# Performance work log

Measured on AMD Instinct MI355X. Metric: run time of the kernel, lower is better.

## Reference

```python
import jax, jax.numpy as jnp
import numpy as np

NUM_HEADS = 8

def _l2norm(t, eps=1e-12):
    # F.normalize(p=2, dim=-1) with eps clamp
    n = jnp.sqrt(jnp.sum(t * t, axis=-1, keepdims=True))
    return t / jnp.maximum(n, eps)

def setup_inputs() -> dict:
    key = jax.random.key(0)
    ks = jax.random.split(key, 4)
    B, N, C = 16, 3136, 768
    x = jax.random.normal(ks[0], (B, N, C), dtype=jnp.float32)
    W_qkv = jax.random.normal(ks[1], (C, 3 * C), dtype=jnp.float32) * (1.0 / np.sqrt(C))
    temp = jnp.ones((NUM_HEADS, 1, 1), dtype=jnp.float32)
    W_proj = jax.random.normal(ks[2], (C, C), dtype=jnp.float32) * (1.0 / np.sqrt(C))
    b_proj = jnp.zeros((C,), dtype=jnp.float32)
    return {"x": x, "W_qkv": W_qkv, "temp": temp, "W_proj": W_proj, "b_proj": b_proj}

def reference(x, W_qkv, temp, W_proj, b_proj):
    B, N, C = x.shape
    h = NUM_HEADS
    d = C // h
    qkv = (x @ W_qkv).reshape(B, N, 3, h, d)
    qkv = jnp.transpose(qkv, (2, 0, 3, 1, 4))  # [3,B,h,N,d]
    q, k, v = qkv[0], qkv[1], qkv[2]           # [B,h,N,d]
    # transpose to channel-major: [B,h,d,N]
    q = jnp.swapaxes(q, -2, -1)
    k = jnp.swapaxes(k, -2, -1)
    v = jnp.swapaxes(v, -2, -1)
    q = _l2norm(q)
    k = _l2norm(k)
    # attn = k @ q^T over token dim: [B,h,d,d]
    attn = jnp.einsum('bhcn,bhen->bhce', k, q)
    attn = attn * temp  # temp broadcasts [h,1,1]
    attn = jax.nn.softmax(attn, axis=-1)
    out = jnp.einsum('bhce,bhen->bhcn', attn, v)  # [B,h,d,N]
    out = jnp.transpose(out, (0, 3, 1, 2)).reshape(B, N, C)
    return out @ W_proj + b_proj
```

## Files before the change

### kernel.cpp

```cpp
#include <hip/hip_runtime.h>

using bf16x8 = __attribute__((ext_vector_type(8))) __bf16;
using f32x4  = __attribute__((ext_vector_type(4))) float;

#define AS1 __attribute__((address_space(1)))
#define AS3 __attribute__((address_space(3)))

__device__ __forceinline__ unsigned short f2bf(float f) {
    unsigned int x = __float_as_uint(f);
    x += 0x7fffu + ((x >> 16) & 1u);
    return (unsigned short)(x >> 16);
}

__device__ __forceinline__ int xcd_remap(int orig, int nwg) {
    int q = nwg >> 3, r = nwg & 7;
    int xcd = orig & 7, lin = orig >> 3;
    return (xcd < r ? xcd * (q + 1) : r * (q + 1) + (xcd - r) * q) + lin;
}

__global__ void cvt_f32_bf16_kernel(const float4* __restrict__ in, ushort4* __restrict__ out, int n4) {
    int stride = gridDim.x * blockDim.x;
    for (int i = blockIdx.x * blockDim.x + threadIdx.x; i < n4; i += stride) {
        float4 v = in[i];
        ushort4 o;
        o.x = f2bf(v.x); o.y = f2bf(v.y); o.z = f2bf(v.z); o.w = f2bf(v.w);
        out[i] = o;
    }
}

__global__ void transpose_f32_bf16_kernel(const float* __restrict__ W, unsigned short* __restrict__ Wt,
                                          int K, int N) {
    __shared__ float tile[32][33];
    int n0 = blockIdx.x << 5, k0 = blockIdx.y << 5;
    int tx = threadIdx.x, ty = threadIdx.y;
#pragma unroll
    for (int i = 0; i < 32; i += 8)
        tile[ty + i][tx] = W[(size_t)(k0 + ty + i) * N + (n0 + tx)];
    __syncthreads();
#pragma unroll
    for (int i = 0; i < 32; i += 8)
        Wt[(size_t)(n0 + ty + i) * K + (k0 + tx)] = f2bf(tile[tx][ty + i]);
}

__device__ __forceinline__ void stage_tile_128x64(const unsigned short* g, int ldK,
                                                  unsigned short* lds, int tid) {
#pragma unroll
    for (int r = 0; r < 4; ++r) {
        int i = (r << 8) + tid;
        int row = i >> 3;
        int colb = (i & 7) << 4;
        int srcb = row * (ldK << 1) + (colb ^ ((row & 7) << 4));
        __builtin_amdgcn_global_load_lds(
            (AS1 unsigned int*)(unsigned long long)((const char*)g + srcb),
            (AS3 unsigned int*)((char*)lds + (i << 4)),
            16, 0, 0);
    }
}

__device__ __forceinline__ bf16x8 lds_read_swz(const unsigned short* base, int row, int kbyte) {
    int off = (row << 7) + (kbyte ^ ((row & 7) << 4));
    return *(const bf16x8*)((const char*)base + off);
}

__global__ __launch_bounds__(256, 2)
void gemm_bt_kernel(const unsigned short* __restrict__ A, const unsigned short* __restrict__ Bt,
                    unsigned short* __restrict__ obf, int M, int N, int K, int ntx) {
    __shared__ unsigned short As[128 * 64];
    __shared__ unsigned short Bs[128 * 64];
    int tid = threadIdx.x;
    int lane = tid & 63, w = tid >> 6;
    int wm = w >> 1, wn = w & 1;
    int wg = xcd_remap(blockIdx.x, gridDim.x);
    int bx = wg % ntx, by = wg / ntx;
    int m0 = by << 7, n0 = bx << 7;
    const unsigned short* Ag = A + (size_t)m0 * K;
    const unsigned short* Bg = Bt + (size_t)n0 * K;

    f32x4 zz = {0.f, 0.f, 0.f, 0.f};
    f32x4 acc[4][4];
#pragma unroll
    for (int a = 0; a < 4; ++a)
#pragma unroll
        for (int b = 0; b < 4; ++b) acc[a][b] = zz;

    for (int kb = 0; kb < K; kb += 64) {
        stage_tile_128x64(Ag + kb, K, As, tid);
        stage_tile_128x64(Bg + kb, K, Bs, tid);
        __syncthreads();
#pragma unroll
        for (int ks = 0; ks < 2; ++ks) {
            int kbyte = (ks << 6) + ((lane >> 4) << 4);
            bf16x8 af[4], bfr[4];
#pragma unroll
            for (int f = 0; f < 4; ++f)
                af[f] = lds_read_swz(As, (wm << 6) + (f << 4) + (lane & 15), kbyte);
#pragma unroll
            for (int f = 0; f < 4; ++f)
                bfr[f] = lds_read_swz(Bs, (wn << 6) + (f << 4) + (lane & 15), kbyte);
#pragma unroll
            for (int fm = 0; fm < 4; ++fm)
#pragma unroll
                for (int fn = 0; fn < 4; ++fn)
                    acc[fm][fn] = __builtin_amdgcn_mfma_f32_16x16x32_bf16(af[fm], bfr[fn], acc[fm][fn], 0, 0, 0);
        }
        __syncthreads();
    }

    int rbase = m0 + (wm << 6) + ((lane >> 4) << 2);
    int cbase = n0 + (wn << 6) + (lane & 15);
#pragma unroll
    for (int fm = 0; fm < 4; ++fm)
#pragma unroll
        for (int j = 0; j < 4; ++j) {
            size_t ro = (size_t)(rbase + (fm << 4) + j) * N;
#pragma unroll
            for (int fn = 0; fn < 4; ++fn)
                obf[ro + cbase + (fn << 4)] = f2bf(acc[fm][fn][j]);
        }
}

__global__ __launch_bounds__(256, 2)
void gemm_v_proj_kernel(const unsigned short* __restrict__ qkv, const unsigned short* __restrict__ MT,
                        float* __restrict__ out, const float* __restrict__ bias) {
    __shared__ unsigned short As[128 * 64];
    __shared__ unsigned short Bs[128 * 64];
    int tid = threadIdx.x;
    int lane = tid & 63, w = tid >> 6;
    int wm = w >> 1, wn = w & 1;
    int wg = xcd_remap(blockIdx.x, gridDim.x);
    int bx = wg % 6;
    int t2 = wg / 6;
    int mt = t2 % 25, b = t2 / 25;
    int m0 = mt << 7, n0 = bx << 7;
    const unsigned short* Ab = qkv + (size_t)b * 3136 * 2304 + 1536;
    const unsigned short* Bg = MT + (size_t)b * 589824 + (size_t)n0 * 768;

    f32x4 zz = {0.f, 0.f, 0.f, 0.f};
    f32x4 acc[4][4];
#pragma unroll
    for (int a = 0; a < 4; ++a)
#pragma unroll
        for (int c = 0; c < 4; ++c) acc[a][c] = zz;

    for (int kb = 0; kb < 768; kb += 64) {
#pragma unroll
        for (int r = 0; r < 4; ++r) {
            int i = (r << 8) + tid;
            int row = i >> 3, slot = i & 7;
            int rg = m0 + row; if (rg > 3135) rg = 3135;
            const char* src = (const char*)(Ab + (size_t)rg * 2304 + kb) + ((slot ^ (row & 7)) << 4);
            __builtin_amdgcn_global_load_lds(
                (AS1 unsigned int*)(unsigned long long)src,
                (AS3 unsigned int*)((char*)As + (i << 4)), 16, 0, 0);
        }
        stage_tile_128x64(Bg + kb, 768, Bs, tid);
        __syncthreads();
#pragma unroll
        for (int ks = 0; ks < 2; ++ks) {
            int kbyte = (ks << 6) + ((lane >> 4) << 4);
            bf16x8 af[4], bfr[4];
#pragma unroll
            for (int f = 0; f < 4; ++f)
                af[f] = lds_read_swz(As, (wm << 6) + (f << 4) + (lane & 15), kbyte);
#pragma unroll
            for (int f = 0; f < 4; ++f)
                bfr[f] = lds_read_swz(Bs, (wn << 6) + (f << 4) + (lane & 15), kbyte);
#pragma unroll
            for (int fm = 0; fm < 4; ++fm)
#pragma unroll
                for (int fn = 0; fn < 4; ++fn)
                    acc[fm][fn] = __builtin_amdgcn_mfma_f32_16x16x32_bf16(af[fm], bfr[fn], acc[fm][fn], 0, 0, 0);
        }
        __syncthreads();
    }

    int rloc = m0 + (wm << 6) + ((lane >> 4) << 2);
    int cbase = n0 + (wn << 6) + (lane & 15);
    float bv[4];
#pragma unroll
    for (int fn = 0; fn < 4; ++fn) bv[fn] = bias[cbase + (fn << 4)];
#pragma unroll
    for (int fm = 0; fm < 4; ++fm)
#pragma unroll
        for (int j = 0; j < 4; ++j) {
            int rr = rloc + (fm << 4) + j;
            if (rr < 3136) {
                size_t ro = ((size_t)b * 3136 + rr) * 768;
#pragma unroll
                for (int fn = 0; fn < 4; ++fn)
                    out[ro + cbase + (fn << 4)] = acc[fm][fn][j] + bv[fn];
            }
        }
}

__global__ __launch_bounds__(256)
void cov_mfma_kernel(const unsigned short* __restrict__ qkv, float* __restrict__ S,
                     float* __restrict__ qn2, float* __restrict__ kn2) {
    __shared__ unsigned short Kl[96 * 40];
    __shared__ unsigned short Ql[96 * 40];
    int bh = blockIdx.x;
    int b = bh >> 3, h = bh & 7;
    int tok0 = blockIdx.y * 448;
    int tid = threadIdx.x;
    int lane = tid & 63, w = tid >> 6;
    int wr = w & 1, wc = w >> 1;
    int rot = tid & 7;

    f32x4 zz = {0.f, 0.f, 0.f, 0.f};
    f32x4 acc[3][3];
#pragma unroll
    for (int a = 0; a < 3; ++a)
#pragma unroll
        for (int c = 0; c < 3; ++c) acc[a][c] = zz;
    float qn = 0.f, kn = 0.f;

    const uint4* qg = (const uint4*)qkv;

    for (int step = 0; step < 14; ++step) {
        int tokBase = b * 3136 + tok0 + (step << 5);
        __syncthreads();
#pragma unroll
        for (int r = 0; r < 3; ++r) {
            int idx = (r << 8) + tid;
            int isK = idx >= 384;
            int j = isK ? idx - 384 : idx;
            int tok = j / 12, c = j % 12;
            uint4 u = qg[(size_t)(tokBase + tok) * 288 + h * 12 + (isK ? 96 : 0) + c];
            unsigned short* dst = isK ? Kl : Ql;
            const unsigned short* us = (const unsigned short*)&u;
#pragma unroll
            for (int i = 0; i < 8; ++i) {
                int e = (i + rot) & 7;
                dst[(c * 8 + e) * 40 + tok] = us[e];
            }
        }
        __syncthreads();
        if (tid < 96) {
#pragma unroll
            for (int t = 0; t < 4; ++t) {
                bf16x8 v = *(const bf16x8*)((const char*)Ql + tid * 80 + (t << 4));
#pragma unroll
                for (int i = 0; i < 8; ++i) { float f = (float)v[i]; qn = fmaf(f, f, qn); }
            }
        } else if (tid >= 128 && tid < 224) {
            int c = tid - 128;
#pragma unroll
            for (int t = 0; t < 4; ++t) {
                bf16x8 v = *(const bf16x8*)((const char*)Kl + c * 80 + (t << 4));
#pragma unroll
                for (int i = 0; i < 8; ++i) { float f = (float)v[i]; kn = fmaf(f, f, kn); }
            }
        }
        int kbyte = (lane >> 4) << 4;
        bf16x8 af[3], bfv[3];
#pragma unroll
        for (int f = 0; f < 3; ++f)
            af[f] = *(const bf16x8*)((const char*)Kl + (wr * 48 + f * 16 + (lane & 15)) * 80 + kbyte);
#pragma unroll
        for (int f = 0; f < 3; ++f)
            bfv[f] = *(const bf16x8*)((const char*)Ql + (wc * 48 + f * 16 + (lane & 15)) * 80 + kbyte);
#pragma unroll
        for (int fm = 0; fm < 3; ++fm)
#pragma unroll
            for (int fn = 0; fn < 3; ++fn)
                acc[fm][fn] = __builtin_amdgcn_mfma_f32_16x16x32_bf16(af[fm], bfv[fn], acc[fm][fn], 0, 0, 0);
    }

    float* Sb = S + (size_t)bh * 9216;
    int rloc = wr * 48 + ((lane >> 4) << 2);
    int cloc = wc * 48 + (lane & 15);
#pragma unroll
    for (int fm = 0; fm < 3; ++fm)
#pragma unroll
        for (int fn = 0; fn < 3; ++fn)
#pragma unroll
            for (int j = 0; j < 4; ++j)
                atomicAdd(&Sb[(rloc + fm * 16 + j) * 96 + cloc + fn * 16], acc[fm][fn][j]);
    if (tid < 96) atomicAdd(&qn2[bh * 96 + tid], qn);
    if (tid >= 128 && tid < 224) atomicAdd(&kn2[bh * 96 + tid - 128], kn);
}

__global__ __launch_bounds__(128)
void softmax_kernel(const float* __restrict__ S, const float* __restrict__ qn2,
                    const float* __restrict__ kn2, const float* __restrict__ temp,
                    unsigned short* __restrict__ attnT) {
    int bh = blockIdx.x, h = bh & 7;
    __shared__ float Sl[96 * 97];
    __shared__ float qinv[96];
    int tid = threadIdx.x;
    const float* Sg = S + (size_t)bh * 9216;
    for (int i = tid; i < 9216; i += 128) Sl[(i / 96) * 97 + (i % 96)] = Sg[i];
    if (tid < 96) qinv[tid] = 1.f / fmaxf(sqrtf(qn2[bh * 96 + tid]), 1e-12f);
    __syncthreads();
    if (tid < 96) {
        int c = tid;
        float scale = (1.f / fmaxf(sqrtf(kn2[bh * 96 + c]), 1e-12f)) * temp[h];
        float* row = &Sl[c * 97];
        float mx = -3.4e38f;
        for (int e = 0; e < 96; ++e) {
            float v = row[e] * scale * qinv[e];
            row[e] = v;
            mx = fmaxf(mx, v);
        }
        float s = 0.f;
        for (int e = 0; e < 96; ++e) {
            float p = __expf(row[e] - mx);
            row[e] = p;
            s += p;
        }
        float inv = 1.f / s;
        unsigned short* ab = attnT + (size_t)bh * 9216;
        for (int e = 0; e < 96; ++e) ab[e * 96 + c] = f2bf(row[e] * inv);
    }
}

__global__ __launch_bounds__(256)
void attn_M_kernel(const unsigned short* __restrict__ attnT, const unsigned short* __restrict__ wprojt,
                   unsigned short* __restrict__ MT) {
    int bh = blockIdx.x >> 2, oc = blockIdx.x & 3;
    int b = bh >> 3, h = bh & 7;
    int tid = threadIdx.x, lane = tid & 63, w = tid >> 6;
    int o0 = oc * 192 + w * 48;
    const unsigned short* At = attnT + (size_t)bh * 9216;

    f32x4 zz = {0.f, 0.f, 0.f, 0.f};
    f32x4 acc[6][3];
#pragma unroll
    for (int f = 0; f < 6; ++f)
#pragma unroll
        for (int g = 0; g < 3; ++g) acc[f][g] = zz;

#pragma unroll
    for (int ks = 0; ks < 3; ++ks) {
        int koff = ks * 32 + ((lane >> 4) << 3);
        bf16x8 a[6], bb[3];
#pragma unroll
        for (int f = 0; f < 6; ++f)
            a[f] = *(const bf16x8*)(At + (size_t)(f * 16 + (lane & 15)) * 96 + koff);
#pragma unroll
        for (int g = 0; g < 3; ++g)
            bb[g] = *(const bf16x8*)(wprojt + (size_t)(o0 + g * 16 + (lane & 15)) * 768 + h * 96 + koff);
#pragma unroll
        for (int f = 0; f < 6; ++f)
#pragma unroll
            for (int g = 0; g < 3; ++g)
                acc[f][g] = __builtin_amdgcn_mfma_f32_16x16x32_bf16(a[f], bb[g], acc[f][g], 0, 0, 0);
    }

#pragma unroll
    for (int f = 0; f < 6; ++f)
#pragma unroll
        for (int g = 0; g < 3; ++g) {
            int e = f * 16 + ((lane >> 4) << 2);
            int o = o0 + g * 16 + (lane & 15);
            ushort4 pk;
            pk.x = f2bf(acc[f][g][0]); pk.y = f2bf(acc[f][g][1]);
            pk.z = f2bf(acc[f][g][2]); pk.w = f2bf(acc[f][g][3]);
            *(ushort4*)&MT[((size_t)b * 768 + o) * 768 + h * 96 + e] = pk;
        }
}

extern "C" void kernel_launch(void* const* d_in, const int* in_sizes, int n_in,
                              void* d_out, int out_size, void* d_ws, size_t ws_size,
                              hipStream_t stream) {
    const float* x     = (const float*)d_in[0];
    const float* Wqkv  = (const float*)d_in[1];
    const float* temp  = (const float*)d_in[2];
    const float* Wproj = (const float*)d_in[3];
    const float* bproj = (const float*)d_in[4];
    float* out = (float*)d_out;
    char* ws = (char*)d_ws;

    unsigned short* xbf    = (unsigned short*)(ws);
    unsigned short* qkvbf  = (unsigned short*)(ws + 77070336);
    unsigned short* wqkvt  = (unsigned short*)(ws + 308281344);
    unsigned short* wprojt = (unsigned short*)(ws + 311820288);
    float*          Sbuf   = (float*)        (ws + 312999936);
    float*          qn2    = (float*)        (ws + 317718528);
    float*          kn2    = (float*)        (ws + 317767680);
    unsigned short* attnT  = (unsigned short*)(ws + 317816832);
    unsigned short* MT     = xbf;

    hipMemsetAsync(Sbuf, 0, 4718592 + 49152 + 49152, stream);

    cvt_f32_bf16_kernel<<<2048, 256, 0, stream>>>((const float4*)x, (ushort4*)xbf, 38535168 / 4);
    transpose_f32_bf16_kernel<<<dim3(72, 24), dim3(32, 8), 0, stream>>>(Wqkv, wqkvt, 768, 2304);
    transpose_f32_bf16_kernel<<<dim3(24, 24), dim3(32, 8), 0, stream>>>(Wproj, wprojt, 768, 768);

    gemm_bt_kernel<<<392 * 18, 256, 0, stream>>>(xbf, wqkvt, qkvbf, 50176, 2304, 768, 18);
    cov_mfma_kernel<<<dim3(128, 7), 256, 0, stream>>>(qkvbf, Sbuf, qn2, kn2);
    softmax_kernel<<<128, 128, 0, stream>>>(Sbuf, qn2, kn2, temp, attnT);
    attn_M_kernel<<<512, 256, 0, stream>>>(attnT, wprojt, MT);
    gemm_v_proj_kernel<<<2400, 256, 0, stream>>>(qkvbf, MT, out, bproj);
}
```

Before: 412.8 us.

## Replace both GEMMs with a double-buffered 256x256 eight-wave phased MFMA kernel

Both the QKV projection and the V/proj GEMM now use one templated kernel with 256x256 tiles, 512 threads, and double-buffered LDS (128KB). The next K-tile's global-to-LDS loads are issued in the middle of the MFMA phases, with explicit barriers, waitcnts and setprio, so memory latency overlaps compute. Larger tiles raise data reuse per block, but they leave fewer blocks in the grid, especially for the per-batch second GEMM, where 3136 rows do not divide evenly into 256-row tiles. The very large LDS footprint also limits occupancy.

```diff
diff --git a/kernel.cpp b/kernel.cpp
--- a/kernel.cpp
+++ b/kernel.cpp
@@ -5,6 +5,11 @@
 
 #define AS1 __attribute__((address_space(1)))
 #define AS3 __attribute__((address_space(3)))
+
+#define SB()     __builtin_amdgcn_s_barrier()
+#define LGKM0()  asm volatile("s_waitcnt lgkmcnt(0)")
+#define VM0()    asm volatile("s_waitcnt vmcnt(0)")
+#define SCHED0() __builtin_amdgcn_sched_barrier(0)
 
 __device__ __forceinline__ unsigned short f2bf(float f) {
     unsigned int x = __float_as_uint(f);
@@ -42,155 +47,148 @@
         Wt[(size_t)(n0 + ty + i) * K + (k0 + tx)] = f2bf(tile[tx][ty + i]);
 }
 
-__device__ __forceinline__ void stage_tile_128x64(const unsigned short* g, int ldK,
-                                                  unsigned short* lds, int tid) {
+__device__ __forceinline__ bf16x8 lds_read_swz(const char* base, int row, int ks, int lane) {
+    int kbyte = (ks << 6) + ((lane >> 4) << 4);
+    int off = (row << 7) + (kbyte ^ ((row & 7) << 4));
+    return *(const bf16x8*)(base + off);
+}
+
+__device__ __forceinline__ void stage256x64(const unsigned short* g, int ldaE, int Mcap,
+                                            char* dst, int tid) {
 #pragma unroll
     for (int r = 0; r < 4; ++r) {
-        int i = (r << 8) + tid;
-        int row = i >> 3;
-        int colb = (i & 7) << 4;
-        int srcb = row * (ldK << 1) + (colb ^ ((row & 7) << 4));
+        int i = (r << 9) + tid;
+        int row = i >> 3, slot = i & 7;
+        int rg = row < Mcap ? row : Mcap - 1;
+        size_t srcb = (size_t)rg * ((size_t)ldaE << 1) + ((slot ^ (row & 7)) << 4);
         __builtin_amdgcn_global_load_lds(
             (AS1 unsigned int*)(unsigned long long)((const char*)g + srcb),
-            (AS3 unsigned int*)((char*)lds + (i << 4)),
-            16, 0, 0);
-    }
-}
-
-__device__ __forceinline__ bf16x8 lds_read_swz(const unsigned short* base, int row, int kbyte) {
-    int off = (row << 7) + (kbyte ^ ((row & 7) << 4));
-    return *(const bf16x8*)((const char*)base + off);
-}
-
-__global__ __launch_bounds__(256, 2)
-void gemm_bt_kernel(const unsigned short* __restrict__ A, const unsigned short* __restrict__ Bt,
-                    unsigned short* __restrict__ obf, int M, int N, int K, int ntx) {
-    __shared__ unsigned short As[128 * 64];
-    __shared__ unsigned short Bs[128 * 64];
-    int tid = threadIdx.x;
-    int lane = tid & 63, w = tid >> 6;
-    int wm = w >> 1, wn = w & 1;
+            (AS3 unsigned int*)(dst + (i << 4)), 16, 0, 0);
+    }
+}
+
+template <int OUTMODE>
+__global__ __launch_bounds__(512, 2)
+void gemm256_8ph(const unsigned short* __restrict__ A, const unsigned short* __restrict__ Bt,
+                 unsigned short* __restrict__ obf, float* __restrict__ of32,
+                 const float* __restrict__ bias,
+                 int K, int lda, int Nld, int nbx, int nmt, int Mrows,
+                 long strideA, long strideB, long strideO) {
+    __shared__ char smem[131072];
+    int tid = threadIdx.x, lane = tid & 63, w = tid >> 6;
+    int wm = w >> 2, wn = w & 3;
+    int l15 = lane & 15;
+
     int wg = xcd_remap(blockIdx.x, gridDim.x);
-    int bx = wg % ntx, by = wg / ntx;
-    int m0 = by << 7, n0 = bx << 7;
-    const unsigned short* Ag = A + (size_t)m0 * K;
-    const unsigned short* Bg = Bt + (size_t)n0 * K;
+    int bx = wg % nbx; int r1 = wg / nbx; int mt = r1 % nmt; int b = r1 / nmt;
+    int m0 = mt << 8, n0 = bx << 8;
+    int Mcap = Mrows - m0; if (Mcap > 256) Mcap = 256;
+    const unsigned short* Ag = A + (long)b * strideA + (size_t)m0 * lda;
+    const unsigned short* Bg = Bt + (long)b * strideB + (size_t)n0 * K;
+    int nkt = K >> 6;
 
     f32x4 zz = {0.f, 0.f, 0.f, 0.f};
-    f32x4 acc[4][4];
-#pragma unroll
-    for (int a = 0; a < 4; ++a)
-#pragma unroll
-        for (int b = 0; b < 4; ++b) acc[a][b] = zz;
-
-    for (int kb = 0; kb < K; kb += 64) {
-        stage_tile_128x64(Ag + kb, K, As, tid);
-        stage_tile_128x64(Bg + kb, K, Bs, tid);
-        __syncthreads();
-#pragma unroll
-        for (int ks = 0; ks < 2; ++ks) {
-            int kbyte = (ks << 6) + ((lane >> 4) << 4);
-            bf16x8 af[4], bfr[4];
-#pragma unroll
-            for (int f = 0; f < 4; ++f)
-                af[f] = lds_read_swz(As, (wm << 6) + (f << 4) + (lane & 15), kbyte);
-#pragma unroll
-            for (int f = 0; f < 4; ++f)
-                bfr[f] = lds_read_swz(Bs, (wn << 6) + (f << 4) + (lane & 15), kbyte);
-#pragma unroll
-            for (int fm = 0; fm < 4; ++fm)
+    f32x4 acc[8][4];
+#pragma unroll
+    for (int a = 0; a < 8; ++a)
+#pragma unroll
+        for (int c = 0; c < 4; ++c) acc[a][c] = zz;
+
+    stage256x64(Ag, lda, Mcap, smem, tid);
+    stage256x64(Bg, K, 256, smem + 32768, tid);
+    VM0();
+    SB(); SCHED0();
+
+    for (int t = 0; t < nkt; ++t) {
+        const char* Ab = smem + ((t & 1) << 16);
+        const char* Bb = Ab + 32768;
+        char* An = smem + (((t + 1) & 1) << 16);
+        int arow = (wm << 7) + l15;
+        int brow = (wn << 6) + l15;
+
+        bf16x8 aF[4], aG[4], bL[4], bH[4];
+#pragma unroll
+        for (int f = 0; f < 4; ++f) aF[f] = lds_read_swz(Ab, arow + (f << 4), 0, lane);
+#pragma unroll
+        for (int f = 0; f < 4; ++f) bL[f] = lds_read_swz(Bb, brow + (f << 4), 0, lane);
+        if (t + 1 < nkt) stage256x64(Ag + ((t + 1) << 6), lda, Mcap, An, tid);
+        SB(); LGKM0(); SCHED0();
+        __builtin_amdgcn_s_setprio(1);
+#pragma unroll
+        for (int fm = 0; fm < 4; ++fm)
+#pragma unroll
+            for (int fn = 0; fn < 4; ++fn)
+                acc[fm][fn] = __builtin_amdgcn_mfma_f32_16x16x32_bf16(aF[fm], bL[fn], acc[fm][fn], 0, 0, 0);
+        __builtin_amdgcn_s_setprio(0);
+        SB(); SCHED0();
+#pragma unroll
+        for (int f = 0; f < 4; ++f) aG[f] = lds_read_swz(Ab, arow + 64 + (f << 4), 0, lane);
+        if (t + 1 < nkt) stage256x64(Bg + ((t + 1) << 6), K, 256, An + 32768, tid);
+        SB(); LGKM0(); SCHED0();
+        __builtin_amdgcn_s_setprio(1);
+#pragma unroll
+        for (int fm = 0; fm < 4; ++fm)
+#pragma unroll
+            for (int fn = 0; fn < 4; ++fn)
+                acc[fm + 4][fn] = __builtin_amdgcn_mfma_f32_16x16x32_bf16(aG[fm], bL[fn], acc[fm + 4][fn], 0, 0, 0);
+        __builtin_amdgcn_s_setprio(0);
+        SB(); SCHED0();
+#pragma unroll
+        for (int f = 0; f < 4; ++f) aF[f] = lds_read_swz(Ab, arow + (f << 4), 1, lane);
+#pragma unroll
+        for (int f = 0; f < 4; ++f) bH[f] = lds_read_swz(Bb, brow + (f << 4), 1, lane);
+        SB(); LGKM0(); SCHED0();
+        __builtin_amdgcn_s_setprio(1);
+#pragma unroll
+        for (int fm = 0; fm < 4; ++fm)
+#pragma unroll
+            for (int fn = 0; fn < 4; ++fn)
+                acc[fm][fn] = __builtin_amdgcn_mfma_f32_16x16x32_bf16(aF[fm], bH[fn], acc[fm][fn], 0, 0, 0);
+        __builtin_amdgcn_s_setprio(0);
+        SB(); SCHED0();
+#pragma unroll
+        for (int f = 0; f < 4; ++f) aG[f] = lds_read_swz(Ab, arow + 64 + (f << 4), 1, lane);
+        SB(); LGKM0(); SCHED0();
+        __builtin_amdgcn_s_setprio(1);
+#pragma unroll
+        for (int fm = 0; fm < 4; ++fm)
+#pragma unroll
+            for (int fn = 0; fn < 4; ++fn)
+                acc[fm + 4][fn] = __builtin_amdgcn_mfma_f32_16x16x32_bf16(aG[fm], bH[fn], acc[fm + 4][fn], 0, 0, 0);
+        __builtin_amdgcn_s_setprio(0);
+        if (t + 1 < nkt) VM0();
+        SB(); SCHED0();
+    }
+
+    int rbase = m0 + (wm << 7) + ((lane >> 4) << 2);
+    int cbase = n0 + (wn << 6) + l15;
+    if (OUTMODE == 0) {
+#pragma unroll
+        for (int fm = 0; fm < 8; ++fm)
+#pragma unroll
+            for (int j = 0; j < 4; ++j) {
+                size_t ro = (size_t)(rbase + (fm << 4) + j) * Nld;
 #pragma unroll
                 for (int fn = 0; fn < 4; ++fn)
-                    acc[fm][fn] = __builtin_amdgcn_mfma_f32_16x16x32_bf16(af[fm], bfr[fn], acc[fm][fn], 0, 0, 0);
-        }
-        __syncthreads();
-    }
-
-    int rbase = m0 + (wm << 6) + ((lane >> 4) << 2);
-    int cbase = n0 + (wn << 6) + (lane & 15);
-#pragma unroll
-    for (int fm = 0; fm < 4; ++fm)
-#pragma unroll
-        for (int j = 0; j < 4; ++j) {
-            size_t ro = (size_t)(rbase + (fm << 4) + j) * N;
-#pragma unroll
-            for (int fn = 0; fn < 4; ++fn)
-                obf[ro + cbase + (fn << 4)] = f2bf(acc[fm][fn][j]);
-        }
-}
-
-__global__ __launch_bounds__(256, 2)
-void gemm_v_proj_kernel(const unsigned short* __restrict__ qkv, const unsigned short* __restrict__ MT,
-                        float* __restrict__ out, const float* __restrict__ bias) {
-    __shared__ unsigned short As[128 * 64];
-    __shared__ unsigned short Bs[128 * 64];
-    int tid = threadIdx.x;
-    int lane = tid & 63, w = tid >> 6;
-    int wm = w >> 1, wn = w & 1;
-    int wg = xcd_remap(blockIdx.x, gridDim.x);
-    int bx = wg % 6;
-    int t2 = wg / 6;
-    int mt = t2 % 25, b = t2 / 25;
-    int m0 = mt << 7, n0 = bx << 7;
-    const unsigned short* Ab = qkv + (size_t)b * 3136 * 2304 + 1536;
-    const unsigned short* Bg = MT + (size_t)b * 589824 + (size_t)n0 * 768;
-
-    f32x4 zz = {0.f, 0.f, 0.f, 0.f};
-    f32x4 acc[4][4];
-#pragma unroll
-    for (int a = 0; a < 4; ++a)
-#pragma unroll
-        for (int c = 0; c < 4; ++c) acc[a][c] = zz;
-
-    for (int kb = 0; kb < 768; kb += 64) {
-#pragma unroll
-        for (int r = 0; r < 4; ++r) {
-            int i = (r << 8) + tid;
-            int row = i >> 3, slot = i & 7;
-            int rg = m0 + row; if (rg > 3135) rg = 3135;
-            const char* src = (const char*)(Ab + (size_t)rg * 2304 + kb) + ((slot ^ (row & 7)) << 4);
-            __builtin_amdgcn_global_load_lds(
-                (AS1 unsigned int*)(unsigned long long)src,
-                (AS3 unsigned int*)((char*)As + (i << 4)), 16, 0, 0);
-        }
-        stage_tile_128x64(Bg + kb, 768, Bs, tid);
-        __syncthreads();
-#pragma unroll
-        for (int ks = 0; ks < 2; ++ks) {
-            int kbyte = (ks << 6) + ((lane >> 4) << 4);
-            bf16x8 af[4], bfr[4];
-#pragma unroll
-            for (int f = 0; f < 4; ++f)
-                af[f] = lds_read_swz(As, (wm << 6) + (f << 4) + (lane & 15), kbyte);
-#pragma unroll
-            for (int f = 0; f < 4; ++f)
-                bfr[f] = lds_read_swz(Bs, (wn << 6) + (f << 4) + (lane & 15), kbyte);
-#pragma unroll
-            for (int fm = 0; fm < 4; ++fm)
-#pragma unroll
-                for (int fn = 0; fn < 4; ++fn)
-                    acc[fm][fn] = __builtin_amdgcn_mfma_f32_16x16x32_bf16(af[fm], bfr[fn], acc[fm][fn], 0, 0, 0);
-        }
-        __syncthreads();
-    }
-
-    int rloc = m0 + (wm << 6) + ((lane >> 4) << 2);
-    int cbase = n0 + (wn << 6) + (lane & 15);
-    float bv[4];
-#pragma unroll
-    for (int fn = 0; fn < 4; ++fn) bv[fn] = bias[cbase + (fn << 4)];
-#pragma unroll
-    for (int fm = 0; fm < 4; ++fm)
-#pragma unroll
-        for (int j = 0; j < 4; ++j) {
-            int rr = rloc + (fm << 4) + j;
-            if (rr < 3136) {
-                size_t ro = ((size_t)b * 3136 + rr) * 768;
-#pragma unroll
-                for (int fn = 0; fn < 4; ++fn)
-                    out[ro + cbase + (fn << 4)] = acc[fm][fn][j] + bv[fn];
-            }
-        }
+                    obf[ro + cbase + (fn << 4)] = f2bf(acc[fm][fn][j]);
+            }
+    } else {
+        float bv[4];
+#pragma unroll
+        for (int fn = 0; fn < 4; ++fn) bv[fn] = bias[cbase + (fn << 4)];
+#pragma unroll
+        for (int fm = 0; fm < 8; ++fm)
+#pragma unroll
+            for (int j = 0; j < 4; ++j) {
+                int rr = rbase + (fm << 4) + j;
+                if (rr < Mrows) {
+                    size_t ro = (long)b * strideO + (size_t)rr * Nld;
+#pragma unroll
+                    for (int fn = 0; fn < 4; ++fn)
+                        of32[ro + cbase + (fn << 4)] = acc[fm][fn][j] + bv[fn];
+                }
+            }
+    }
 }
 
 __global__ __launch_bounds__(256)
@@ -387,9 +385,12 @@
     transpose_f32_bf16_kernel<<<dim3(72, 24), dim3(32, 8), 0, stream>>>(Wqkv, wqkvt, 768, 2304);
     transpose_f32_bf16_kernel<<<dim3(24, 24), dim3(32, 8), 0, stream>>>(Wproj, wprojt, 768, 768);
 
-    gemm_bt_kernel<<<392 * 18, 256, 0, stream>>>(xbf, wqkvt, qkvbf, 50176, 2304, 768, 18);
+    gemm256_8ph<0><<<196 * 9, 512, 0, stream>>>(xbf, wqkvt, qkvbf, nullptr, nullptr,
+                                                768, 768, 2304, 9, 196, 50176, 0, 0, 0);
     cov_mfma_kernel<<<dim3(128, 7), 256, 0, stream>>>(qkvbf, Sbuf, qn2, kn2);
     softmax_kernel<<<128, 128, 0, stream>>>(Sbuf, qn2, kn2, temp, attnT);
     attn_M_kernel<<<512, 256, 0, stream>>>(attnT, wprojt, MT);
-    gemm_v_proj_kernel<<<2400, 256, 0, stream>>>(qkvbf, MT, out, bproj);
-}
+    gemm256_8ph<1><<<16 * 13 * 3, 512, 0, stream>>>(qkvbf + 1536, MT, nullptr, out, bproj,
+                                                    768, 2304, 768, 3, 13, 3136,
+                                                    7225344L, 589824L, 2408448L);
+}
```

New measurement: 431.2 us. 1.04x slower.
